# Optimization experiments

Hardware: AMD Instinct MI355X
Metric: run time of the kernel (lower is better)

The kernel has to match this reference:

```python
import jax, jax.numpy as jnp
import numpy as np

N_NODES = 100000
N_EDGES = 1600000
D_IN, D_HID, D_OUT = 128, 128, 64


def setup_inputs() -> dict:
    key = jax.random.key(0)
    ks = jax.random.split(key, 10)
    scale = 0.05
    return {
        "x": jax.random.normal(ks[0], (N_NODES, D_IN), jnp.float32),
        "edge_index": jax.random.randint(ks[1], (2, N_EDGES), 0, N_NODES, dtype=jnp.int64),
        "edge_weight": jax.random.uniform(ks[2], (N_EDGES,), jnp.float32),
        "W1": jax.random.normal(ks[3], (D_IN, D_HID), jnp.float32) * scale,
        "b1": jnp.zeros((D_HID,), jnp.float32),
        "W2": jax.random.normal(ks[4], (D_HID, D_HID), jnp.float32) * scale,
        "b2": jnp.zeros((D_HID,), jnp.float32),
        "W3": jax.random.normal(ks[5], (D_HID, D_OUT), jnp.float32) * scale,
        "b3": jnp.zeros((D_OUT,), jnp.float32),
    }


def reference(x, edge_index, edge_weight, W1, b1, W2, b2, W3, b3):
    N = x.shape[0]
    # GCN normalization with self-loops (PyG gcn_norm, add_self_loops=True, fill=1)
    loop = jnp.arange(N)
    row = jnp.concatenate([edge_index[0], loop])  # source nodes
    col = jnp.concatenate([edge_index[1], loop])  # target nodes
    w = jnp.concatenate([edge_weight, jnp.ones((N,), x.dtype)])
    deg = jax.ops.segment_sum(w, col, num_segments=N)
    dinv = jnp.where(deg > 0, jax.lax.rsqrt(deg), 0.0)
    norm = dinv[row] * w * dinv[col]  # [E+N]

    def gcn_conv(h, W, b):
        h = h @ W                                   # dense linear transform
        msg = h[row] * norm[:, None]                # gather + normalize
        return jax.ops.segment_sum(msg, col, num_segments=N) + b  # scatter-add

    h = jax.nn.relu(gcn_conv(x, W1, b1))   # dropout = identity (eval mode)
    h = jax.nn.relu(gcn_conv(h, W2, b2))
    return gcn_conv(h, W3, b3)
```

## Files before the change

### kernel.cpp

```cpp
#include <hip/hip_runtime.h>
#include <hip/hip_bf16.h>


static inline size_t align_up(size_t x, size_t a) { return (x + a - 1) & ~(a - 1); }

typedef _Float16 half8 __attribute__((ext_vector_type(8)));
typedef float f32x4 __attribute__((ext_vector_type(4)));

#define BSTRIDE 64

__device__ inline float2 h2_unpack(unsigned u) {
    union { unsigned u; _Float16 h[2]; } c; c.u = u;
    return make_float2((float)c.h[0], (float)c.h[1]);
}
__device__ inline unsigned h2_pack(float a, float b) {
    union { unsigned u; _Float16 h[2]; } c;
    c.h[0] = (_Float16)a; c.h[1] = (_Float16)b;
    return c.u;
}
__device__ inline float ent_w(unsigned v) {
    union { unsigned short s; _Float16 h; } c;
    c.s = (unsigned short)(v & 0x7FFFu);
    return (float)c.h;
}


__global__ void k_setup(unsigned long long* __restrict__ packed, int N,
                        const float* __restrict__ W1, _Float16* __restrict__ Wt1,
                        const float* __restrict__ W2, _Float16* __restrict__ Wt2,
                        const float* __restrict__ W3, _Float16* __restrict__ Wt3) {
    int i = blockIdx.x * blockDim.x + threadIdx.x;
    if (i < N) packed[i] = 0ull;
    if (i < 128 * 128) {
        int k = i >> 7, n = i & 127;
        Wt1[(size_t)n * 128 + k] = (_Float16)W1[i];
        Wt2[(size_t)n * 128 + k] = (_Float16)W2[i];
    }
    if (i < 128 * 64) {
        int k = i / 64, n = i % 64;
        Wt3[(size_t)n * 128 + k] = (_Float16)W3[i];
    }
}

__global__ void k_rank_scatter(const int* __restrict__ row, const int* __restrict__ col,
                               const float* __restrict__ w,
                               unsigned long long* __restrict__ packed,
                               unsigned* __restrict__ ent, int E) {
    int e = blockIdx.x * blockDim.x + threadIdx.x;
    if (e < E) {
        int c = col[e];
        float wf = w[e];
        unsigned long long add =
            (1ull << 40) | (unsigned long long)(wf * 16777216.0f);
        unsigned long long old = atomicAdd(&packed[c], add);
        unsigned rank = (unsigned)(old >> 40);
        if (rank < BSTRIDE) {
            union { _Float16 h; unsigned short s; } cv; cv.h = (_Float16)wf;
            ent[(size_t)c * BSTRIDE + rank] =
                ((unsigned)row[e] << 15) | (cv.s & 0x7FFFu);
        }
    }
}

__global__ void k_dinv(const unsigned long long* __restrict__ packed,
                       float* __restrict__ dinv, int N) {
    int i = blockIdx.x * blockDim.x + threadIdx.x;
    if (i < N) {
        unsigned long long p = packed[i];
        float deg = 1.0f + (float)(p & ((1ull << 40) - 1)) * (1.0f / 16777216.0f);
        dinv[i] = rsqrtf(deg);
    }
}


template <int NF, bool A_FP32>
__global__ __launch_bounds__(256) void k_gemm_mfma(
    const void* __restrict__ Aptr, const _Float16* __restrict__ Wt,
    const float* __restrict__ dinv, _Float16* __restrict__ G, int M) {
    const int K = 128;
    const int N = NF * 16;
    const int lane = threadIdx.x & 63;
    const int wv = threadIdx.x >> 6;
    const int mbase = blockIdx.x * 64 + wv * 16;
    const int r = lane & 15;
    const int g = lane >> 4;
    const int mrow = mbase + r;
    const int mc = (mrow < M) ? mrow : (M - 1);

    half8 a[4];
    if (A_FP32) {
        const float* A = (const float*)Aptr;
#pragma unroll
        for (int ks = 0; ks < 4; ++ks) {
            const float* p = A + (size_t)mc * K + ks * 32 + g * 8;
            float4 lo = *reinterpret_cast<const float4*>(p);
            float4 hi = *reinterpret_cast<const float4*>(p + 4);
            half8 h;
            h[0] = (_Float16)lo.x; h[1] = (_Float16)lo.y;
            h[2] = (_Float16)lo.z; h[3] = (_Float16)lo.w;
            h[4] = (_Float16)hi.x; h[5] = (_Float16)hi.y;
            h[6] = (_Float16)hi.z; h[7] = (_Float16)hi.w;
            a[ks] = h;
        }
    } else {
        const _Float16* A = (const _Float16*)Aptr;
#pragma unroll
        for (int ks = 0; ks < 4; ++ks)
            a[ks] = *reinterpret_cast<const half8*>(A + (size_t)mc * K + ks * 32 + g * 8);
    }

    f32x4 acc[NF];
#pragma unroll
    for (int nf = 0; nf < NF; ++nf) acc[nf] = (f32x4){0.f, 0.f, 0.f, 0.f};

#pragma unroll
    for (int nf = 0; nf < NF; ++nf) {
        const _Float16* wp = Wt + (size_t)(nf * 16 + r) * K + g * 8;
#pragma unroll
        for (int ks = 0; ks < 4; ++ks) {
            half8 b = *reinterpret_cast<const half8*>(wp + ks * 32);
            acc[nf] = __builtin_amdgcn_mfma_f32_16x16x32_f16(a[ks], b, acc[nf], 0, 0, 0);
        }
    }

#pragma unroll
    for (int reg = 0; reg < 4; ++reg) {
        int row = mbase + g * 4 + reg;
        if (row < M) {
            float di = dinv[row];
#pragma unroll
            for (int nf = 0; nf < NF; ++nf)
                G[(size_t)row * N + nf * 16 + r] = (_Float16)(acc[nf][reg] * di);
        }
    }
}


template <bool RELU, bool OUT16>
__global__ __launch_bounds__(256) void k_agg128(
    const _Float16* __restrict__ G, const unsigned long long* __restrict__ packed,
    const unsigned* __restrict__ ent, const float* __restrict__ dinv,
    const float* __restrict__ bias, void* __restrict__ Hout, int M) {
    const int lane = threadIdx.x & 63;
    const int wid = blockIdx.x * (blockDim.x >> 6) + (threadIdx.x >> 6);
    const int nw = gridDim.x * (blockDim.x >> 6);
    const float bx = bias[lane * 2];
    const float by = bias[lane * 2 + 1];
    const unsigned* Gu = reinterpret_cast<const unsigned*>(G);

    for (int i = wid; i < M; i += nw) {
        unsigned long long p = packed[i];
        int cnt = (int)(p >> 40); cnt = (cnt > BSTRIDE) ? BSTRIDE : cnt;
        const unsigned* eb = ent + (size_t)i * BSTRIDE;
        float2 self = h2_unpack(Gu[(size_t)i * 64 + lane]);
        float ax0 = self.x, ax1 = 0.f, ax2 = 0.f, ax3 = 0.f;
        float ay0 = self.y, ay1 = 0.f, ay2 = 0.f, ay3 = 0.f;
        for (int j = 0; j < cnt; j += 8) {
            unsigned v0, v1, v2, v3, v4, v5, v6, v7;
            {
                int l = cnt - 1;
                int j1 = j + 1, j2 = j + 2, j3 = j + 3;
                int j4 = j + 4, j5 = j + 5, j6 = j + 6, j7 = j + 7;
                v0 = eb[j];
                v1 = eb[j1 < cnt ? j1 : l]; v2 = eb[j2 < cnt ? j2 : l];
                v3 = eb[j3 < cnt ? j3 : l]; v4 = eb[j4 < cnt ? j4 : l];
                v5 = eb[j5 < cnt ? j5 : l]; v6 = eb[j6 < cnt ? j6 : l];
                v7 = eb[j7 < cnt ? j7 : l];
                if (j1 >= cnt) v1 &= ~0x7FFFu; if (j2 >= cnt) v2 &= ~0x7FFFu;
                if (j3 >= cnt) v3 &= ~0x7FFFu; if (j4 >= cnt) v4 &= ~0x7FFFu;
                if (j5 >= cnt) v5 &= ~0x7FFFu; if (j6 >= cnt) v6 &= ~0x7FFFu;
                if (j7 >= cnt) v7 &= ~0x7FFFu;
            }
            const unsigned* Gl = Gu + lane;
            unsigned u0 = Gl[(size_t)(v0 >> 15) * 64];
            unsigned u1 = Gl[(size_t)(v1 >> 15) * 64];
            unsigned u2 = Gl[(size_t)(v2 >> 15) * 64];
            unsigned u3 = Gl[(size_t)(v3 >> 15) * 64];
            unsigned u4 = Gl[(size_t)(v4 >> 15) * 64];
            unsigned u5 = Gl[(size_t)(v5 >> 15) * 64];
            unsigned u6 = Gl[(size_t)(v6 >> 15) * 64];
            unsigned u7 = Gl[(size_t)(v7 >> 15) * 64];
            float w0 = ent_w(v0), w1 = ent_w(v1), w2 = ent_w(v2), w3 = ent_w(v3);
            float w4 = ent_w(v4), w5 = ent_w(v5), w6 = ent_w(v6), w7 = ent_w(v7);
            float2 g0 = h2_unpack(u0), g1 = h2_unpack(u1);
            float2 g2 = h2_unpack(u2), g3 = h2_unpack(u3);
            float2 g4 = h2_unpack(u4), g5 = h2_unpack(u5);
            float2 g6 = h2_unpack(u6), g7 = h2_unpack(u7);
            ax0 = fmaf(w0, g0.x, ax0); ay0 = fmaf(w0, g0.y, ay0);
            ax1 = fmaf(w1, g1.x, ax1); ay1 = fmaf(w1, g1.y, ay1);
            ax2 = fmaf(w2, g2.x, ax2); ay2 = fmaf(w2, g2.y, ay2);
            ax3 = fmaf(w3, g3.x, ax3); ay3 = fmaf(w3, g3.y, ay3);
            ax0 = fmaf(w4, g4.x, ax0); ay0 = fmaf(w4, g4.y, ay0);
            ax1 = fmaf(w5, g5.x, ax1); ay1 = fmaf(w5, g5.y, ay1);
            ax2 = fmaf(w6, g6.x, ax2); ay2 = fmaf(w6, g6.y, ay2);
            ax3 = fmaf(w7, g7.x, ax3); ay3 = fmaf(w7, g7.y, ay3);
        }
        float accx = (ax0 + ax1) + (ax2 + ax3);
        float accy = (ay0 + ay1) + (ay2 + ay3);
        float di = dinv[i];
        float ox = fmaf(di, accx, bx);
        float oy = fmaf(di, accy, by);
        if (RELU) { ox = fmaxf(ox, 0.f); oy = fmaxf(oy, 0.f); }
        if (OUT16) {
            ((unsigned*)Hout)[(size_t)i * 64 + lane] = h2_pack(ox, oy);
        } else {
            *reinterpret_cast<float2*>((float*)Hout + (size_t)i * 128 + lane * 2)
                = make_float2(ox, oy);
        }
    }
}


__global__ __launch_bounds__(256) void k_agg64(
    const _Float16* __restrict__ G, const unsigned long long* __restrict__ packed,
    const unsigned* __restrict__ ent, const float* __restrict__ dinv,
    const float* __restrict__ bias, float* __restrict__ Hout, int M) {
    const int lane = threadIdx.x & 63;
    const int sub = lane >> 5;
    const int ln = lane & 31;
    const int wid = blockIdx.x * (blockDim.x >> 6) + (threadIdx.x >> 6);
    const int nw = gridDim.x * (blockDim.x >> 6);
    const float bx = bias[ln * 2];
    const float by = bias[ln * 2 + 1];
    const unsigned* Gu = reinterpret_cast<const unsigned*>(G);

    for (int base = wid * 2; base < M; base += nw * 2) {
        int i = base + sub;
        bool valid = (i < M);
        if (!valid) i = M - 1;
        unsigned long long p = packed[i];
        int cnt = (int)(p >> 40); cnt = (cnt > BSTRIDE) ? BSTRIDE : cnt;
        const unsigned* eb = ent + (size_t)i * BSTRIDE;
        float2 self = h2_unpack(Gu[(size_t)i * 32 + ln]);
        float ax0 = self.x, ax1 = 0.f, ax2 = 0.f, ax3 = 0.f;
        float ay0 = self.y, ay1 = 0.f, ay2 = 0.f, ay3 = 0.f;
        for (int j = 0; j < cnt; j += 8) {
            unsigned v0, v1, v2, v3, v4, v5, v6, v7;
            {
                int l = cnt - 1;
                int j1 = j + 1, j2 = j + 2, j3 = j + 3;
                int j4 = j + 4, j5 = j + 5, j6 = j + 6, j7 = j + 7;
                v0 = eb[j];
                v1 = eb[j1 < cnt ? j1 : l]; v2 = eb[j2 < cnt ? j2 : l];
                v3 = eb[j3 < cnt ? j3 : l]; v4 = eb[j4 < cnt ? j4 : l];
                v5 = eb[j5 < cnt ? j5 : l]; v6 = eb[j6 < cnt ? j6 : l];
                v7 = eb[j7 < cnt ? j7 : l];
                if (j1 >= cnt) v1 &= ~0x7FFFu; if (j2 >= cnt) v2 &= ~0x7FFFu;
                if (j3 >= cnt) v3 &= ~0x7FFFu; if (j4 >= cnt) v4 &= ~0x7FFFu;
                if (j5 >= cnt) v5 &= ~0x7FFFu; if (j6 >= cnt) v6 &= ~0x7FFFu;
                if (j7 >= cnt) v7 &= ~0x7FFFu;
            }
            const unsigned* Gl = Gu + ln;
            unsigned u0 = Gl[(size_t)(v0 >> 15) * 32];
            unsigned u1 = Gl[(size_t)(v1 >> 15) * 32];
            unsigned u2 = Gl[(size_t)(v2 >> 15) * 32];
            unsigned u3 = Gl[(size_t)(v3 >> 15) * 32];
            unsigned u4 = Gl[(size_t)(v4 >> 15) * 32];
            unsigned u5 = Gl[(size_t)(v5 >> 15) * 32];
            unsigned u6 = Gl[(size_t)(v6 >> 15) * 32];
            unsigned u7 = Gl[(size_t)(v7 >> 15) * 32];
            float w0 = ent_w(v0), w1 = ent_w(v1), w2 = ent_w(v2), w3 = ent_w(v3);
            float w4 = ent_w(v4), w5 = ent_w(v5), w6 = ent_w(v6), w7 = ent_w(v7);
            float2 g0 = h2_unpack(u0), g1 = h2_unpack(u1);
            float2 g2 = h2_unpack(u2), g3 = h2_unpack(u3);
            float2 g4 = h2_unpack(u4), g5 = h2_unpack(u5);
            float2 g6 = h2_unpack(u6), g7 = h2_unpack(u7);
            ax0 = fmaf(w0, g0.x, ax0); ay0 = fmaf(w0, g0.y, ay0);
            ax1 = fmaf(w1, g1.x, ax1); ay1 = fmaf(w1, g1.y, ay1);
            ax2 = fmaf(w2, g2.x, ax2); ay2 = fmaf(w2, g2.y, ay2);
            ax3 = fmaf(w3, g3.x, ax3); ay3 = fmaf(w3, g3.y, ay3);
            ax0 = fmaf(w4, g4.x, ax0); ay0 = fmaf(w4, g4.y, ay0);
            ax1 = fmaf(w5, g5.x, ax1); ay1 = fmaf(w5, g5.y, ay1);
            ax2 = fmaf(w6, g6.x, ax2); ay2 = fmaf(w6, g6.y, ay2);
            ax3 = fmaf(w7, g7.x, ax3); ay3 = fmaf(w7, g7.y, ay3);
        }
        float accx = (ax0 + ax1) + (ax2 + ax3);
        float accy = (ay0 + ay1) + (ay2 + ay3);
        float di = dinv[i];
        if (valid) {
            *reinterpret_cast<float2*>(Hout + (size_t)i * 64 + ln * 2)
                = make_float2(fmaf(di, accx, bx), fmaf(di, accy, by));
        }
    }
}


extern "C" void kernel_launch(void* const* d_in, const int* in_sizes, int n_in,
                              void* d_out, int out_size, void* d_ws, size_t ws_size,
                              hipStream_t stream) {
    const float* x  = (const float*)d_in[0];
    const int*   ei = (const int*)d_in[1];
    const float* ew = (const float*)d_in[2];
    const float* W1 = (const float*)d_in[3];
    const float* b1 = (const float*)d_in[4];
    const float* W2 = (const float*)d_in[5];
    const float* b2 = (const float*)d_in[6];
    const float* W3 = (const float*)d_in[7];
    const float* b3 = (const float*)d_in[8];
    float* out = (float*)d_out;

    const int DIN = 128, DHID = 128, DOUT = 64;
    const int N = in_sizes[0] / DIN;
    const int E = in_sizes[2];
    const int* e_row = ei;
    const int* e_col = ei + E;

    char* ws = (char*)d_ws;
    size_t off = 0;
    unsigned long long* packed = (unsigned long long*)(ws + off); off = align_up(off + (size_t)N * 8, 256);
    float* dinv   = (float*)(ws + off);    off = align_up(off + (size_t)N * 4, 256);
    unsigned* ent = (unsigned*)(ws + off); off = align_up(off + (size_t)N * BSTRIDE * 4, 256);
    _Float16* gbuf = (_Float16*)(ws + off); off = align_up(off + (size_t)N * DHID * 2, 256);
    _Float16* hbuf = (_Float16*)(ws + off); off = align_up(off + (size_t)N * DHID * 2, 256);
    _Float16* Wt1 = (_Float16*)(ws + off); off = align_up(off + (size_t)128 * 128 * 2, 256);
    _Float16* Wt2 = (_Float16*)(ws + off); off = align_up(off + (size_t)128 * 128 * 2, 256);
    _Float16* Wt3 = (_Float16*)(ws + off); off = align_up(off + (size_t)128 * 64 * 2, 256);
    (void)ws_size;

    const int nbN = (N + 255) / 256;
    const int nbE = (E + 255) / 256;

    k_setup<<<nbN, 256, 0, stream>>>(packed, N, W1, Wt1, W2, Wt2, W3, Wt3);
    k_rank_scatter<<<nbE, 256, 0, stream>>>(e_row, e_col, ew, packed, ent, E);
    k_dinv<<<nbN, 256, 0, stream>>>(packed, dinv, N);

    const int gemm_blocks = (N + 63) / 64;
    const int agg_blocks = 4096;

    k_gemm_mfma<8, true><<<gemm_blocks, 256, 0, stream>>>(x, Wt1, dinv, gbuf, N);
    k_agg128<true, true><<<agg_blocks, 256, 0, stream>>>(gbuf, packed, ent, dinv, b1, hbuf, N);

    k_gemm_mfma<8, false><<<gemm_blocks, 256, 0, stream>>>(hbuf, Wt2, dinv, gbuf, N);
    k_agg128<true, true><<<agg_blocks, 256, 0, stream>>>(gbuf, packed, ent, dinv, b2, hbuf, N);

    k_gemm_mfma<4, false><<<gemm_blocks, 256, 0, stream>>>(hbuf, Wt3, dinv, gbuf, N);
    k_agg64<<<agg_blocks, 256, 0, stream>>>(gbuf, packed, ent, dinv, b3, out, N);

    (void)n_in; (void)out_size;
}
```

Before: 383.0 us.

## Build deterministic bucketed adjacency via chunked LDS histogram, scan, and scatter

Replaces the global 64-bit atomic rank-scatter with a two-pass scheme. Per-chunk, per-node-partition histograms are built in shared memory, a per-node exclusive scan runs over chunks, and a second pass scatters edges using shared-memory atomics at the scanned offsets. Degree is recomputed from fp16 weights with a wavefront reduction. The aggregation kernels also switch to 16-wide unrolled gathers with an unconditional first batch. The aim is to remove global-atomic contention and raise memory-level parallelism in the gathers, at the cost of extra passes over the edge list, a 32xN histogram buffer, and wasted loads for low-degree nodes. Computing degree from fp16 weights and dropping edges beyond 64 per node also slightly changes normalization precision.

Result: slower. 474.7 us (+23.9%).

```diff
diff --git a/kernel.cpp b/kernel.cpp
--- a/kernel.cpp
+++ b/kernel.cpp
@@ -8,6 +8,8 @@
 typedef float f32x4 __attribute__((ext_vector_type(4)));
 
 #define BSTRIDE 64
+#define NCHUNK  32
+#define PART_MAX 12544
 
 __device__ inline float2 h2_unpack(unsigned u) {
     union { unsigned u; _Float16 h[2]; } c; c.u = u;
@@ -25,12 +27,10 @@
 }
 
 
-__global__ void k_setup(unsigned long long* __restrict__ packed, int N,
-                        const float* __restrict__ W1, _Float16* __restrict__ Wt1,
+__global__ void k_setup(const float* __restrict__ W1, _Float16* __restrict__ Wt1,
                         const float* __restrict__ W2, _Float16* __restrict__ Wt2,
                         const float* __restrict__ W3, _Float16* __restrict__ Wt3) {
     int i = blockIdx.x * blockDim.x + threadIdx.x;
-    if (i < N) packed[i] = 0ull;
     if (i < 128 * 128) {
         int k = i >> 7, n = i & 127;
         Wt1[(size_t)n * 128 + k] = (_Float16)W1[i];
@@ -42,34 +42,87 @@
     }
 }
 
-__global__ void k_rank_scatter(const int* __restrict__ row, const int* __restrict__ col,
-                               const float* __restrict__ w,
-                               unsigned long long* __restrict__ packed,
-                               unsigned* __restrict__ ent, int E) {
-    int e = blockIdx.x * blockDim.x + threadIdx.x;
-    if (e < E) {
+__global__ __launch_bounds__(256) void k_hist(
+    const int* __restrict__ col, unsigned* __restrict__ hist,
+    int E, int N, int chunk) {
+    const int t = blockIdx.x & 7;
+    const int k = blockIdx.x >> 3;
+    const int part = (N + 7) >> 3;
+    const int c0 = t * part;
+    const int c1 = (c0 + part < N) ? c0 + part : N;
+    const int psz = c1 - c0;
+    __shared__ unsigned h[PART_MAX];
+    for (int i = threadIdx.x; i < psz; i += 256) h[i] = 0;
+    __syncthreads();
+    const int e0 = k * chunk;
+    const int e1 = (e0 + chunk < E) ? e0 + chunk : E;
+    for (int e = e0 + threadIdx.x; e < e1; e += 256) {
         int c = col[e];
-        float wf = w[e];
-        unsigned long long add =
-            (1ull << 40) | (unsigned long long)(wf * 16777216.0f);
-        unsigned long long old = atomicAdd(&packed[c], add);
-        unsigned rank = (unsigned)(old >> 40);
-        if (rank < BSTRIDE) {
-            union { _Float16 h; unsigned short s; } cv; cv.h = (_Float16)wf;
-            ent[(size_t)c * BSTRIDE + rank] =
-                ((unsigned)row[e] << 15) | (cv.s & 0x7FFFu);
-        }
-    }
-}
-
-__global__ void k_dinv(const unsigned long long* __restrict__ packed,
-                       float* __restrict__ dinv, int N) {
-    int i = blockIdx.x * blockDim.x + threadIdx.x;
-    if (i < N) {
-        unsigned long long p = packed[i];
-        float deg = 1.0f + (float)(p & ((1ull << 40) - 1)) * (1.0f / 16777216.0f);
-        dinv[i] = rsqrtf(deg);
-    }
+        if (c >= c0 && c < c1) atomicAdd(&h[c - c0], 1u);
+    }
+    __syncthreads();
+    for (int i = threadIdx.x; i < psz; i += 256)
+        hist[(size_t)k * N + c0 + i] = h[i];
+}
+
+__global__ void k_scan(unsigned* __restrict__ hist, unsigned* __restrict__ cnt, int N) {
+    int c = blockIdx.x * blockDim.x + threadIdx.x;
+    if (c >= N) return;
+    unsigned v[NCHUNK];
+#pragma unroll
+    for (int k = 0; k < NCHUNK; ++k) v[k] = hist[(size_t)k * N + c];
+    unsigned run = 0;
+#pragma unroll
+    for (int k = 0; k < NCHUNK; ++k) {
+        hist[(size_t)k * N + c] = run;
+        run += v[k];
+    }
+    cnt[c] = run;
+}
+
+__global__ __launch_bounds__(256) void k_scatter2(
+    const int* __restrict__ row, const int* __restrict__ col,
+    const float* __restrict__ w, const unsigned* __restrict__ hist,
+    unsigned* __restrict__ ent, int E, int N, int chunk) {
+    const int t = blockIdx.x & 7;
+    const int k = blockIdx.x >> 3;
+    const int part = (N + 7) >> 3;
+    const int c0 = t * part;
+    const int c1 = (c0 + part < N) ? c0 + part : N;
+    const int psz = c1 - c0;
+    __shared__ unsigned cur[PART_MAX];
+    for (int i = threadIdx.x; i < psz; i += 256)
+        cur[i] = hist[(size_t)k * N + c0 + i];
+    __syncthreads();
+    const int e0 = k * chunk;
+    const int e1 = (e0 + chunk < E) ? e0 + chunk : E;
+    for (int e = e0 + threadIdx.x; e < e1; e += 256) {
+        int c = col[e];
+        if (c >= c0 && c < c1) {
+            unsigned r = atomicAdd(&cur[c - c0], 1u);
+            if (r < BSTRIDE) {
+                union { _Float16 h; unsigned short s; } cv;
+                cv.h = (_Float16)w[e];
+                ent[(size_t)c * BSTRIDE + r] =
+                    ((unsigned)row[e] << 15) | (cv.s & 0x7FFFu);
+            }
+        }
+    }
+}
+
+__global__ __launch_bounds__(256) void k_dinv2(
+    const unsigned* __restrict__ ent, const unsigned* __restrict__ cnt,
+    float* __restrict__ dinv, int M) {
+    const int lane = threadIdx.x & 63;
+    const int i = (blockIdx.x * blockDim.x + threadIdx.x) >> 6;
+    if (i >= M) return;
+    int c = cnt[i]; c = (c > BSTRIDE) ? BSTRIDE : c;
+    unsigned v = ent[(size_t)i * BSTRIDE + lane];
+    float wv = (lane < c) ? ent_w(v) : 0.0f;
+#pragma unroll
+    for (int off = 1; off < 64; off <<= 1)
+        wv += __shfl_xor(wv, off, 64);
+    if (lane == 0) dinv[i] = rsqrtf(1.0f + wv);
 }
 
 
@@ -138,7 +191,7 @@
 
 template <bool RELU, bool OUT16>
 __global__ __launch_bounds__(256) void k_agg128(
-    const _Float16* __restrict__ G, const unsigned long long* __restrict__ packed,
+    const _Float16* __restrict__ G, const unsigned* __restrict__ cnt,
     const unsigned* __restrict__ ent, const float* __restrict__ dinv,
     const float* __restrict__ bias, void* __restrict__ Hout, int M) {
     const int lane = threadIdx.x & 63;
@@ -149,55 +202,56 @@
     const unsigned* Gu = reinterpret_cast<const unsigned*>(G);
 
     for (int i = wid; i < M; i += nw) {
-        unsigned long long p = packed[i];
-        int cnt = (int)(p >> 40); cnt = (cnt > BSTRIDE) ? BSTRIDE : cnt;
         const unsigned* eb = ent + (size_t)i * BSTRIDE;
+        int c = (int)cnt[i]; c = (c > BSTRIDE) ? BSTRIDE : c;
+        float di = dinv[i];
         float2 self = h2_unpack(Gu[(size_t)i * 64 + lane]);
         float ax0 = self.x, ax1 = 0.f, ax2 = 0.f, ax3 = 0.f;
         float ay0 = self.y, ay1 = 0.f, ay2 = 0.f, ay3 = 0.f;
-        for (int j = 0; j < cnt; j += 8) {
-            unsigned v0, v1, v2, v3, v4, v5, v6, v7;
-            {
-                int l = cnt - 1;
-                int j1 = j + 1, j2 = j + 2, j3 = j + 3;
-                int j4 = j + 4, j5 = j + 5, j6 = j + 6, j7 = j + 7;
-                v0 = eb[j];
-                v1 = eb[j1 < cnt ? j1 : l]; v2 = eb[j2 < cnt ? j2 : l];
-                v3 = eb[j3 < cnt ? j3 : l]; v4 = eb[j4 < cnt ? j4 : l];
-                v5 = eb[j5 < cnt ? j5 : l]; v6 = eb[j6 < cnt ? j6 : l];
-                v7 = eb[j7 < cnt ? j7 : l];
-                if (j1 >= cnt) v1 &= ~0x7FFFu; if (j2 >= cnt) v2 &= ~0x7FFFu;
-                if (j3 >= cnt) v3 &= ~0x7FFFu; if (j4 >= cnt) v4 &= ~0x7FFFu;
-                if (j5 >= cnt) v5 &= ~0x7FFFu; if (j6 >= cnt) v6 &= ~0x7FFFu;
-                if (j7 >= cnt) v7 &= ~0x7FFFu;
-            }
-            const unsigned* Gl = Gu + lane;
-            unsigned u0 = Gl[(size_t)(v0 >> 15) * 64];
-            unsigned u1 = Gl[(size_t)(v1 >> 15) * 64];
-            unsigned u2 = Gl[(size_t)(v2 >> 15) * 64];
-            unsigned u3 = Gl[(size_t)(v3 >> 15) * 64];
-            unsigned u4 = Gl[(size_t)(v4 >> 15) * 64];
-            unsigned u5 = Gl[(size_t)(v5 >> 15) * 64];
-            unsigned u6 = Gl[(size_t)(v6 >> 15) * 64];
-            unsigned u7 = Gl[(size_t)(v7 >> 15) * 64];
-            float w0 = ent_w(v0), w1 = ent_w(v1), w2 = ent_w(v2), w3 = ent_w(v3);
-            float w4 = ent_w(v4), w5 = ent_w(v5), w6 = ent_w(v6), w7 = ent_w(v7);
-            float2 g0 = h2_unpack(u0), g1 = h2_unpack(u1);
-            float2 g2 = h2_unpack(u2), g3 = h2_unpack(u3);
-            float2 g4 = h2_unpack(u4), g5 = h2_unpack(u5);
-            float2 g6 = h2_unpack(u6), g7 = h2_unpack(u7);
-            ax0 = fmaf(w0, g0.x, ax0); ay0 = fmaf(w0, g0.y, ay0);
-            ax1 = fmaf(w1, g1.x, ax1); ay1 = fmaf(w1, g1.y, ay1);
-            ax2 = fmaf(w2, g2.x, ax2); ay2 = fmaf(w2, g2.y, ay2);
-            ax3 = fmaf(w3, g3.x, ax3); ay3 = fmaf(w3, g3.y, ay3);
-            ax0 = fmaf(w4, g4.x, ax0); ay0 = fmaf(w4, g4.y, ay0);
-            ax1 = fmaf(w5, g5.x, ax1); ay1 = fmaf(w5, g5.y, ay1);
-            ax2 = fmaf(w6, g6.x, ax2); ay2 = fmaf(w6, g6.y, ay2);
-            ax3 = fmaf(w7, g7.x, ax3); ay3 = fmaf(w7, g7.y, ay3);
+
+        {
+            unsigned v[16];
+#pragma unroll
+            for (int u = 0; u < 16; ++u) v[u] = eb[u];
+            float wg[16];
+#pragma unroll
+            for (int u = 0; u < 16; ++u) wg[u] = (u < c) ? ent_w(v[u]) : 0.f;
+            unsigned gv[16];
+#pragma unroll
+            for (int u = 0; u < 16; ++u) gv[u] = Gu[(size_t)(v[u] >> 15) * 64 + lane];
+#pragma unroll
+            for (int u = 0; u < 16; ++u) {
+                float2 gg = h2_unpack(gv[u]);
+                if ((u & 3) == 0) { ax0 = fmaf(wg[u], gg.x, ax0); ay0 = fmaf(wg[u], gg.y, ay0); }
+                if ((u & 3) == 1) { ax1 = fmaf(wg[u], gg.x, ax1); ay1 = fmaf(wg[u], gg.y, ay1); }
+                if ((u & 3) == 2) { ax2 = fmaf(wg[u], gg.x, ax2); ay2 = fmaf(wg[u], gg.y, ay2); }
+                if ((u & 3) == 3) { ax3 = fmaf(wg[u], gg.x, ax3); ay3 = fmaf(wg[u], gg.y, ay3); }
+            }
+        }
+        for (int j = 16; j < c; j += 16) {
+            unsigned v[16];
+#pragma unroll
+            for (int u = 0; u < 16; ++u) {
+                int idx = j + u; idx = (idx < 63) ? idx : 63;
+                v[u] = eb[idx];
+            }
+            float wg[16];
+#pragma unroll
+            for (int u = 0; u < 16; ++u) wg[u] = (j + u < c) ? ent_w(v[u]) : 0.f;
+            unsigned gv[16];
+#pragma unroll
+            for (int u = 0; u < 16; ++u) gv[u] = Gu[(size_t)(v[u] >> 15) * 64 + lane];
+#pragma unroll
+            for (int u = 0; u < 16; ++u) {
+                float2 gg = h2_unpack(gv[u]);
+                if ((u & 3) == 0) { ax0 = fmaf(wg[u], gg.x, ax0); ay0 = fmaf(wg[u], gg.y, ay0); }
+                if ((u & 3) == 1) { ax1 = fmaf(wg[u], gg.x, ax1); ay1 = fmaf(wg[u], gg.y, ay1); }
+                if ((u & 3) == 2) { ax2 = fmaf(wg[u], gg.x, ax2); ay2 = fmaf(wg[u], gg.y, ay2); }
+                if ((u & 3) == 3) { ax3 = fmaf(wg[u], gg.x, ax3); ay3 = fmaf(wg[u], gg.y, ay3); }
+            }
         }
         float accx = (ax0 + ax1) + (ax2 + ax3);
         float accy = (ay0 + ay1) + (ay2 + ay3);
-        float di = dinv[i];
         float ox = fmaf(di, accx, bx);
         float oy = fmaf(di, accy, by);
         if (RELU) { ox = fmaxf(ox, 0.f); oy = fmaxf(oy, 0.f); }
@@ -212,7 +266,7 @@
 
 
 __global__ __launch_bounds__(256) void k_agg64(
-    const _Float16* __restrict__ G, const unsigned long long* __restrict__ packed,
+    const _Float16* __restrict__ G, const unsigned* __restrict__ cnt,
     const unsigned* __restrict__ ent, const float* __restrict__ dinv,
     const float* __restrict__ bias, float* __restrict__ Hout, int M) {
     const int lane = threadIdx.x & 63;
@@ -228,55 +282,55 @@
         int i = base + sub;
         bool valid = (i < M);
         if (!valid) i = M - 1;
-        unsigned long long p = packed[i];
-        int cnt = (int)(p >> 40); cnt = (cnt > BSTRIDE) ? BSTRIDE : cnt;
         const unsigned* eb = ent + (size_t)i * BSTRIDE;
+        int c = (int)cnt[i]; c = (c > BSTRIDE) ? BSTRIDE : c;
+        float di = dinv[i];
         float2 self = h2_unpack(Gu[(size_t)i * 32 + ln]);
         float ax0 = self.x, ax1 = 0.f, ax2 = 0.f, ax3 = 0.f;
         float ay0 = self.y, ay1 = 0.f, ay2 = 0.f, ay3 = 0.f;
-        for (int j = 0; j < cnt; j += 8) {
-            unsigned v0, v1, v2, v3, v4, v5, v6, v7;
-            {
-                int l = cnt - 1;
-                int j1 = j + 1, j2 = j + 2, j3 = j + 3;
-                int j4 = j + 4, j5 = j + 5, j6 = j + 6, j7 = j + 7;
-                v0 = eb[j];
-                v1 = eb[j1 < cnt ? j1 : l]; v2 = eb[j2 < cnt ? j2 : l];
-                v3 = eb[j3 < cnt ? j3 : l]; v4 = eb[j4 < cnt ? j4 : l];
-                v5 = eb[j5 < cnt ? j5 : l]; v6 = eb[j6 < cnt ? j6 : l];
-                v7 = eb[j7 < cnt ? j7 : l];
-                if (j1 >= cnt) v1 &= ~0x7FFFu; if (j2 >= cnt) v2 &= ~0x7FFFu;
-                if (j3 >= cnt) v3 &= ~0x7FFFu; if (j4 >= cnt) v4 &= ~0x7FFFu;
-                if (j5 >= cnt) v5 &= ~0x7FFFu; if (j6 >= cnt) v6 &= ~0x7FFFu;
-                if (j7 >= cnt) v7 &= ~0x7FFFu;
-            }
-            const unsigned* Gl = Gu + ln;
-            unsigned u0 = Gl[(size_t)(v0 >> 15) * 32];
-            unsigned u1 = Gl[(size_t)(v1 >> 15) * 32];
-            unsigned u2 = Gl[(size_t)(v2 >> 15) * 32];
-            unsigned u3 = Gl[(size_t)(v3 >> 15) * 32];
-            unsigned u4 = Gl[(size_t)(v4 >> 15) * 32];
-            unsigned u5 = Gl[(size_t)(v5 >> 15) * 32];
-            unsigned u6 = Gl[(size_t)(v6 >> 15) * 32];
-            unsigned u7 = Gl[(size_t)(v7 >> 15) * 32];
-            float w0 = ent_w(v0), w1 = ent_w(v1), w2 = ent_w(v2), w3 = ent_w(v3);
-            float w4 = ent_w(v4), w5 = ent_w(v5), w6 = ent_w(v6), w7 = ent_w(v7);
-            float2 g0 = h2_unpack(u0), g1 = h2_unpack(u1);
-            float2 g2 = h2_unpack(u2), g3 = h2_unpack(u3);
-            float2 g4 = h2_unpack(u4), g5 = h2_unpack(u5);
-            float2 g6 = h2_unpack(u6), g7 = h2_unpack(u7);
-            ax0 = fmaf(w0, g0.x, ax0); ay0 = fmaf(w0, g0.y, ay0);
-            ax1 = fmaf(w1, g1.x, ax1); ay1 = fmaf(w1, g1.y, ay1);
-            ax2 = fmaf(w2, g2.x, ax2); ay2 = fmaf(w2, g2.y, ay2);
-            ax3 = fmaf(w3, g3.x, ax3); ay3 = fmaf(w3, g3.y, ay3);
-            ax0 = fmaf(w4, g4.x, ax0); ay0 = fmaf(w4, g4.y, ay0);
-            ax1 = fmaf(w5, g5.x, ax1); ay1 = fmaf(w5, g5.y, ay1);
-            ax2 = fmaf(w6, g6.x, ax2); ay2 = fmaf(w6, g6.y, ay2);
-            ax3 = fmaf(w7, g7.x, ax3); ay3 = fmaf(w7, g7.y, ay3);
+        {
+            unsigned v[16];
+#pragma unroll
+            for (int u = 0; u < 16; ++u) v[u] = eb[u];
+            float wg[16];
+#pragma unroll
+            for (int u = 0; u < 16; ++u) wg[u] = (u < c) ? ent_w(v[u]) : 0.f;
+            unsigned gv[16];
+#pragma unroll
+            for (int u = 0; u < 16; ++u) gv[u] = Gu[(size_t)(v[u] >> 15) * 32 + ln];
+#pragma unroll
+            for (int u = 0; u < 16; ++u) {
+                float2 gg = h2_unpack(gv[u]);
+                if ((u & 3) == 0) { ax0 = fmaf(wg[u], gg.x, ax0); ay0 = fmaf(wg[u], gg.y, ay0); }
+                if ((u & 3) == 1) { ax1 = fmaf(wg[u], gg.x, ax1); ay1 = fmaf(wg[u], gg.y, ay1); }
+                if ((u & 3) == 2) { ax2 = fmaf(wg[u], gg.x, ax2); ay2 = fmaf(wg[u], gg.y, ay2); }
+                if ((u & 3) == 3) { ax3 = fmaf(wg[u], gg.x, ax3); ay3 = fmaf(wg[u], gg.y, ay3); }
+            }
+        }
+        for (int j = 16; j < c; j += 16) {
+            unsigned v[16];
+#pragma unroll
+            for (int u = 0; u < 16; ++u) {
+                int idx = j + u; idx = (idx < 63) ? idx : 63;
+                v[u] = eb[idx];
+            }
+            float wg[16];
+#pragma unroll
+            for (int u = 0; u < 16; ++u) wg[u] = (j + u < c) ? ent_w(v[u]) : 0.f;
+            unsigned gv[16];
+#pragma unroll
+            for (int u = 0; u < 16; ++u) gv[u] = Gu[(size_t)(v[u] >> 15) * 32 + ln];
+#pragma unroll
+            for (int u = 0; u < 16; ++u) {
+                float2 gg = h2_unpack(gv[u]);
+                if ((u & 3) == 0) { ax0 = fmaf(wg[u], gg.x, ax0); ay0 = fmaf(wg[u], gg.y, ay0); }
+                if ((u & 3) == 1) { ax1 = fmaf(wg[u], gg.x, ax1); ay1 = fmaf(wg[u], gg.y, ay1); }
+                if ((u & 3) == 2) { ax2 = fmaf(wg[u], gg.x, ax2); ay2 = fmaf(wg[u], gg.y, ay2); }
+                if ((u & 3) == 3) { ax3 = fmaf(wg[u], gg.x, ax3); ay3 = fmaf(wg[u], gg.y, ay3); }
+            }
         }
         float accx = (ax0 + ax1) + (ax2 + ax3);
         float accy = (ay0 + ay1) + (ay2 + ay3);
-        float di = dinv[i];
         if (valid) {
             *reinterpret_cast<float2*>(Hout + (size_t)i * 64 + ln * 2)
                 = make_float2(fmaf(di, accx, bx), fmaf(di, accy, by));
@@ -307,9 +361,10 @@
 
     char* ws = (char*)d_ws;
     size_t off = 0;
-    unsigned long long* packed = (unsigned long long*)(ws + off); off = align_up(off + (size_t)N * 8, 256);
-    float* dinv   = (float*)(ws + off);    off = align_up(off + (size_t)N * 4, 256);
-    unsigned* ent = (unsigned*)(ws + off); off = align_up(off + (size_t)N * BSTRIDE * 4, 256);
+    unsigned* hist = (unsigned*)(ws + off); off = align_up(off + (size_t)NCHUNK * N * 4, 256);
+    unsigned* cnt  = (unsigned*)(ws + off); off = align_up(off + (size_t)N * 4, 256);
+    float* dinv    = (float*)(ws + off);    off = align_up(off + (size_t)N * 4, 256);
+    unsigned* ent  = (unsigned*)(ws + off); off = align_up(off + (size_t)N * BSTRIDE * 4, 256);
     _Float16* gbuf = (_Float16*)(ws + off); off = align_up(off + (size_t)N * DHID * 2, 256);
     _Float16* hbuf = (_Float16*)(ws + off); off = align_up(off + (size_t)N * DHID * 2, 256);
     _Float16* Wt1 = (_Float16*)(ws + off); off = align_up(off + (size_t)128 * 128 * 2, 256);
@@ -317,24 +372,26 @@
     _Float16* Wt3 = (_Float16*)(ws + off); off = align_up(off + (size_t)128 * 64 * 2, 256);
     (void)ws_size;
 
+    const int chunk = (E + NCHUNK - 1) / NCHUNK;
     const int nbN = (N + 255) / 256;
-    const int nbE = (E + 255) / 256;
-
-    k_setup<<<nbN, 256, 0, stream>>>(packed, N, W1, Wt1, W2, Wt2, W3, Wt3);
-    k_rank_scatter<<<nbE, 256, 0, stream>>>(e_row, e_col, ew, packed, ent, E);
-    k_dinv<<<nbN, 256, 0, stream>>>(packed, dinv, N);
+
+    k_setup<<<(128 * 128 + 255) / 256, 256, 0, stream>>>(W1, Wt1, W2, Wt2, W3, Wt3);
+    k_hist<<<8 * NCHUNK, 256, 0, stream>>>(e_col, hist, E, N, chunk);
+    k_scan<<<nbN, 256, 0, stream>>>(hist, cnt, N);
+    k_scatter2<<<8 * NCHUNK, 256, 0, stream>>>(e_row, e_col, ew, hist, ent, E, N, chunk);
+    k_dinv2<<<(N * 64 + 255) / 256, 256, 0, stream>>>(ent, cnt, dinv, N);
 
     const int gemm_blocks = (N + 63) / 64;
     const int agg_blocks = 4096;
 
     k_gemm_mfma<8, true><<<gemm_blocks, 256, 0, stream>>>(x, Wt1, dinv, gbuf, N);
-    k_agg128<true, true><<<agg_blocks, 256, 0, stream>>>(gbuf, packed, ent, dinv, b1, hbuf, N);
+    k_agg128<true, true><<<agg_blocks, 256, 0, stream>>>(gbuf, cnt, ent, dinv, b1, hbuf, N);
 
     k_gemm_mfma<8, false><<<gemm_blocks, 256, 0, stream>>>(hbuf, Wt2, dinv, gbuf, N);
-    k_agg128<true, true><<<agg_blocks, 256, 0, stream>>>(gbuf, packed, ent, dinv, b2, hbuf, N);
+    k_agg128<true, true><<<agg_blocks, 256, 0, stream>>>(gbuf, cnt, ent, dinv, b2, hbuf, N);
 
     k_gemm_mfma<4, false><<<gemm_blocks, 256, 0, stream>>>(hbuf, Wt3, dinv, gbuf, N);
-    k_agg64<<<agg_blocks, 256, 0, stream>>>(gbuf, packed, ent, dinv, b3, out, N);
+    k_agg64<<<agg_blocks, 256, 0, stream>>>(gbuf, cnt, ent, dinv, b3, out, N);
 
     (void)n_in; (void)out_size;
 }
```
